# Optimization experiments

Measured on AMD Instinct MI355X. Metric: run time of the kernel, lower is better.

## Reference

```python
import jax, jax.numpy as jnp
import numpy as np

PATCH = (9, 7, 5, 3)
DIM = 64
HEAD_DIM = 64
HEADS = 8
HIDDEN = 8
DEPTH = 4
SCALE = (HEAD_DIM / HEADS) ** (-0.5)  # per-head dim = 8
EPS = 1e-5


def setup_inputs() -> dict:
    key = jax.random.key(0)
    ks = jax.random.split(key, 8)
    B = 4096
    x = jax.random.normal(ks[0], (B, PATCH[0] * PATCH[0], DIM), dtype=jnp.float32)
    w_qkv = jax.random.normal(ks[1], (DEPTH, DIM, 3 * HEAD_DIM), dtype=jnp.float32) * 0.05
    b_qkv = jnp.zeros((DEPTH, 3 * HEAD_DIM), dtype=jnp.float32)
    w_o = jax.random.normal(ks[2], (DEPTH, HEAD_DIM, DIM), dtype=jnp.float32) * 0.05
    b_o = jnp.zeros((DEPTH, DIM), dtype=jnp.float32)
    ln1_g = jnp.ones((DEPTH, DIM), dtype=jnp.float32)
    ln1_b = jnp.zeros((DEPTH, DIM), dtype=jnp.float32)
    ln2_g = jnp.ones((DEPTH, DIM), dtype=jnp.float32)
    ln2_b = jnp.zeros((DEPTH, DIM), dtype=jnp.float32)
    w1 = jax.random.normal(ks[3], (DEPTH, DIM, HIDDEN), dtype=jnp.float32) * 0.05
    b1 = jnp.zeros((DEPTH, HIDDEN), dtype=jnp.float32)
    w2 = jax.random.normal(ks[4], (DEPTH, HIDDEN, DIM), dtype=jnp.float32) * 0.05
    b2 = jnp.zeros((DEPTH, DIM), dtype=jnp.float32)
    return {"x": x, "w_qkv": w_qkv, "b_qkv": b_qkv, "w_o": w_o, "b_o": b_o,
            "ln1_g": ln1_g, "ln1_b": ln1_b, "ln2_g": ln2_g, "ln2_b": ln2_b,
            "w1": w1, "b1": b1, "w2": w2, "b2": b2}


def _layernorm(x, g, b):
    m = jnp.mean(x, axis=-1, keepdims=True)
    v = jnp.mean(jnp.square(x - m), axis=-1, keepdims=True)
    return (x - m) * jax.lax.rsqrt(v + EPS) * g + b


def reference(x, w_qkv, b_qkv, w_o, b_o, ln1_g, ln1_b, ln2_g, ln2_b, w1, b1, w2, b2):
    B = x.shape[0]
    for i in range(DEPTH):
        n = x.shape[1]
        # --- attention block (Residual(Layernorm(Encoder))) ---
        y = _layernorm(x, ln1_g[i], ln1_b[i])
        qkv = y @ w_qkv[i] + b_qkv[i]                       # [B, n, 3*HEAD_DIM]
        q, k, v = jnp.split(qkv, 3, axis=-1)
        dh = HEAD_DIM // HEADS                              # 8
        q = q.reshape(B, n, HEADS, dh)
        k = k.reshape(B, n, HEADS, dh)
        v = v.reshape(B, n, HEADS, dh)
        dots = jnp.einsum('bihd,bjhd->bhij', q, k) * SCALE  # [B, H, n, n]
        attn = jax.nn.softmax(dots, axis=-1)
        out = jnp.einsum('bhij,bjhd->bihd', attn, v).reshape(B, n, HEAD_DIM)
        out = out @ w_o[i] + b_o[i]
        x = x + out                                         # dropout = identity (eval)
        # --- feedforward block ---
        y = _layernorm(x, ln2_g[i], ln2_b[i])
        h = jax.nn.gelu(y @ w1[i] + b1[i], approximate=False)
        x = x + h @ w2[i] + b2[i]
        # --- spatial pooling / rearrange ---
        p = PATCH[i]
        xg = x.reshape(B, p, p, DIM)                        # 'b (h w) d -> b h w d'
        if i != DEPTH - 1:
            xg = xg[:, 1:-1, 1:-1, :]                       # crop pool_size=1
            x = xg.reshape(B, (p - 2) * (p - 2), DIM)
        else:
            x = jnp.transpose(xg, (0, 3, 1, 2))             # 'b h w d -> b d h w'
    return x  # [B, 64, 3, 3]
```

## Files before the change

### kernel.cpp

```cpp
#include <hip/hip_runtime.h>
#include <hip/hip_bf16.h>
#include <math.h>

#define NT 512

typedef __attribute__((ext_vector_type(8))) short short8v;
typedef __attribute__((ext_vector_type(4))) short short4v;
typedef __attribute__((ext_vector_type(4))) float f32x4;
typedef __attribute__((ext_vector_type(2))) unsigned uint2v;
typedef __attribute__((ext_vector_type(4))) unsigned uint4v;

__device__ __forceinline__ unsigned short f2bf(float x) {
    unsigned u = __float_as_uint(x);
    unsigned r = ((u >> 16) & 1u) + 0x7FFFu;
    return (unsigned short)((u + r) >> 16);
}
__device__ __forceinline__ unsigned pk2(float a, float b) {
    __hip_bfloat162 h = __float22bfloat162_rn(make_float2(a, b));
    unsigned r;
    __builtin_memcpy(&r, &h, sizeof(r));
    return r;
}
__device__ __forceinline__ short bf1(float a) {
    __hip_bfloat16 h = __float2bfloat16(a);
    short r;
    __builtin_memcpy(&r, &h, sizeof(r));
    return r;
}
__device__ __forceinline__ float exp2fast(float x) {
#if __has_builtin(__builtin_amdgcn_exp2f)
    return __builtin_amdgcn_exp2f(x);
#else
    return exp2f(x);
#endif
}
__device__ __forceinline__ float gelu_f(float x) {
    float x3 = x * x * x;
    float e = exp2fast(-2.3022079f * x - 0.1029432f * x3);
    return x / (1.0f + e);
}
__device__ __forceinline__ f32x4 mfma32(short8v a, short8v b, f32x4 c) {
    return __builtin_amdgcn_mfma_f32_16x16x32_bf16(a, b, c, 0, 0, 0);
}

#define WS_WO 49152
#define WS_W1 65536
#define WS_W2 69632
#define WS_TOT 71680

__global__ __launch_bounds__(256) void prep_kernel(
    const float* __restrict__ w_qkv, const float* __restrict__ w_o,
    const float* __restrict__ w1, const float* __restrict__ w2,
    short* __restrict__ ws)
{
    int idx = blockIdx.x * 256 + threadIdx.x;
    if (idx < WS_WO) {
        int l = idx / 12288, r = idx % 12288, c = r >> 6, d = r & 63;
        ws[idx] = (short)f2bf(w_qkv[l * 12288 + d * 192 + c]);
    } else if (idx < WS_W1) {
        int k = idx - WS_WO; int l = k / 4096, r = k % 4096, c = r >> 6, d = r & 63;
        ws[idx] = (short)f2bf(w_o[l * 4096 + d * 64 + c]);
    } else if (idx < WS_W2) {
        int k = idx - WS_W1; int l = k / 1024, r = k % 1024, j = r >> 6, d = r & 63;
        ws[idx] = (j < 8) ? (short)f2bf(w1[l * 512 + d * 8 + j]) : (short)0;
    } else if (idx < WS_TOT) {
        int k = idx - WS_W2; int l = k / 512, r = k % 512, c = r >> 3, j = r & 7;
        ws[idx] = (short)f2bf(w2[l * 512 + j * 64 + c]);
    }
}

template<int N, int P, int L, bool LAST>
__device__ __forceinline__ void layer_fn(
    float* __restrict__ xs, short* __restrict__ ybf, short* __restrict__ qbf,
    short* __restrict__ kbf, short* __restrict__ vT,
    const short* __restrict__ ws,
    const float* __restrict__ b_qkv, const float* __restrict__ b_o,
    const float* __restrict__ ln1_g, const float* __restrict__ ln1_b,
    const float* __restrict__ ln2_g, const float* __restrict__ ln2_b,
    const float* __restrict__ b1,    const float* __restrict__ b2,
    float* __restrict__ out, int b, int t)
{
    constexpr int Mt = (N + 15) / 16;
    constexpr float SCL2E = 0.51010905835f;
    const int wv = t >> 6, l = t & 63, lr = l & 15, lq = l >> 4;
    short8v zero8 = {};
    f32x4 zero4 = {0.f, 0.f, 0.f, 0.f};

    if (t < 64 * Mt) {
        const int token = t >> 2, part = t & 3, d0 = part * 16;
        short* yrow = ybf + token * 72 + d0;
        if (token < N) {
            const int row = (token / P + L) * 9 + token % P + L;
            const float* xr = xs + row * 68 + d0;
            f32x4 v[4];
            #pragma unroll
            for (int k = 0; k < 4; ++k) v[k] = *(const f32x4*)(xr + 4 * k);
            float s1 = 0.f, s2 = 0.f;
            #pragma unroll
            for (int k = 0; k < 4; ++k)
                #pragma unroll
                for (int e = 0; e < 4; ++e) { s1 += v[k][e]; s2 += v[k][e] * v[k][e]; }
            s1 += __shfl_xor(s1, 1); s2 += __shfl_xor(s2, 1);
            s1 += __shfl_xor(s1, 2); s2 += __shfl_xor(s2, 2);
            const float m = s1 * 0.015625f;
            const float r = rsqrtf(s2 * 0.015625f - m * m + 1e-5f);
            uint4v w0, w1v;
            #pragma unroll
            for (int k = 0; k < 4; ++k) {
                f32x4 g  = *(const f32x4*)&ln1_g[L * 64 + d0 + 4 * k];
                f32x4 bb = *(const f32x4*)&ln1_b[L * 64 + d0 + 4 * k];
                unsigned p0 = pk2((v[k][0]-m)*r*g[0]+bb[0], (v[k][1]-m)*r*g[1]+bb[1]);
                unsigned p1 = pk2((v[k][2]-m)*r*g[2]+bb[2], (v[k][3]-m)*r*g[3]+bb[3]);
                if (k == 0) { w0.x = p0; w0.y = p1; }
                else if (k == 1) { w0.z = p0; w0.w = p1; }
                else if (k == 2) { w1v.x = p0; w1v.y = p1; }
                else { w1v.z = p0; w1v.w = p1; }
            }
            *(uint4v*)yrow = w0;
            *(uint4v*)(yrow + 8) = w1v;
        } else {
            uint4v z = {};
            *(uint4v*)yrow = z;
            *(uint4v*)(yrow + 8) = z;
        }
    }
    __syncthreads();

    {
        const short* wqL = ws + L * 12288;
        for (int u = wv; u < Mt * 12; u += 8) {
            const int mt = u / 12, ct = u - mt * 12;
            const short* yr = &ybf[(16 * mt + lr) * 72 + lq * 8];
            short8v y0 = *(const short8v*)yr, y1 = *(const short8v*)(yr + 32);
            const short* wr = &wqL[(16 * ct + lr) * 64 + lq * 8];
            short8v w0 = *(const short8v*)wr, w1 = *(const short8v*)(wr + 32);
            if (ct < 8) {
                f32x4 acc = mfma32(w0, y0, zero4);
                acc = mfma32(w1, y1, acc);
                f32x4 bq = *(const f32x4*)&b_qkv[L * 192 + 16 * ct + lq * 4];
                const int i = 16 * mt + lr;
                if (ct < 4) {
                    unsigned p0 = pk2((acc[0]+bq[0])*SCL2E, (acc[1]+bq[1])*SCL2E);
                    unsigned p1 = pk2((acc[2]+bq[2])*SCL2E, (acc[3]+bq[3])*SCL2E);
                    unsigned* dst = (unsigned*)&qbf[i * 72 + 16 * ct + lq * 4];
                    dst[0] = p0; dst[1] = p1;
                } else {
                    unsigned p0 = pk2(acc[0]+bq[0], acc[1]+bq[1]);
                    unsigned p1 = pk2(acc[2]+bq[2], acc[3]+bq[3]);
                    unsigned* dst = (unsigned*)&kbf[i * 72 + 16 * (ct - 4) + lq * 4];
                    dst[0] = p0; dst[1] = p1;
                }
            } else {
                f32x4 acc = mfma32(y0, w0, zero4);
                acc = mfma32(y1, w1, acc);
                const int cv = 16 * (ct - 8) + lr;
                const float bias = b_qkv[L * 192 + 128 + cv];
                unsigned p0 = pk2(acc[0]+bias, acc[1]+bias);
                unsigned p1 = pk2(acc[2]+bias, acc[3]+bias);
                unsigned* dst = (unsigned*)&vT[cv * 104 + 16 * mt + lq * 4];
                dst[0] = p0; dst[1] = p1;
            }
        }
    }
    __syncthreads();

    {
        const int h = wv, hh = wv >> 1;
        short8v kf[Mt];
        #pragma unroll
        for (int jt = 0; jt < Mt; ++jt)
            kf[jt] = (l < 16) ? *(const short8v*)&kbf[(16 * jt + lr) * 72 + h * 8] : zero8;
#if __has_builtin(__builtin_amdgcn_mfma_f32_16x16x16bf16_1k)
        short4v vf[Mt];
        #pragma unroll
        for (int jt = 0; jt < Mt; ++jt)
            vf[jt] = *(const short4v*)&vT[(16 * hh + lr) * 104 + 16 * jt + lq * 4];
#else
        constexpr int KS2 = (Mt + 1) / 2;
        short8v vf8[KS2];
        #pragma unroll
        for (int ks = 0; ks < KS2; ++ks)
            vf8[ks] = *(const short8v*)&vT[(16 * hh + lr) * 104 + 32 * ks + lq * 8];
#endif
        for (int mt = 0; mt < Mt; ++mt) {
            short8v bq = (l < 16) ? *(const short8v*)&qbf[(16 * mt + lr) * 72 + h * 8] : zero8;
            f32x4 acc[Mt];
            #pragma unroll
            for (int jt = 0; jt < Mt; ++jt) acc[jt] = mfma32(kf[jt], bq, zero4);
            float psum = 0.f;
            #pragma unroll
            for (int jt = 0; jt < Mt; ++jt) {
                #pragma unroll
                for (int rg = 0; rg < 4; ++rg) {
                    const int j = 16 * jt + lq * 4 + rg;
                    float e = exp2fast(acc[jt][rg]);
                    e = (j < N) ? e : 0.f;
                    acc[jt][rg] = e;
                    psum += e;
                }
            }
            float den = psum + __shfl_xor(psum, 16);
            den += __shfl_xor(den, 32);
            const float dinv = 1.0f / den;
            unsigned pkk[Mt][2];
            #pragma unroll
            for (int jt = 0; jt < Mt; ++jt) {
                pkk[jt][0] = pk2(acc[jt][0] * dinv, acc[jt][1] * dinv);
                pkk[jt][1] = pk2(acc[jt][2] * dinv, acc[jt][3] * dinv);
            }
            f32x4 po = zero4;
#if __has_builtin(__builtin_amdgcn_mfma_f32_16x16x16bf16_1k)
            #pragma unroll
            for (int jt = 0; jt < Mt; ++jt) {
                uint2v pw; pw.x = pkk[jt][0]; pw.y = pkk[jt][1];
                short4v bv = __builtin_bit_cast(short4v, pw);
                po = __builtin_amdgcn_mfma_f32_16x16x16bf16_1k(vf[jt], bv, po, 0, 0, 0);
            }
#else
            #pragma unroll
            for (int ks = 0; ks < KS2; ++ks) {
                const int t1ok = (2 * ks + 1) < Mt;
                unsigned pA0 = pkk[2 * ks][0], pA1 = pkk[2 * ks][1];
                unsigned pB0 = t1ok ? pkk[2 * ks + 1][0] : 0u;
                unsigned pB1 = t1ok ? pkk[2 * ks + 1][1] : 0u;
                int i01 = ((((lq & 1) * 2) * 16) + lr) * 4;
                int i23 = ((((lq & 1) * 2 + 1) * 16) + lr) * 4;
                unsigned w0a = (unsigned)__builtin_amdgcn_ds_bpermute(i01, (int)pA0);
                unsigned w0b = (unsigned)__builtin_amdgcn_ds_bpermute(i01, (int)pB0);
                unsigned w1a = (unsigned)__builtin_amdgcn_ds_bpermute(i01, (int)pA1);
                unsigned w1b = (unsigned)__builtin_amdgcn_ds_bpermute(i01, (int)pB1);
                unsigned w2a = (unsigned)__builtin_amdgcn_ds_bpermute(i23, (int)pA0);
                unsigned w2b = (unsigned)__builtin_amdgcn_ds_bpermute(i23, (int)pB0);
                unsigned w3a = (unsigned)__builtin_amdgcn_ds_bpermute(i23, (int)pA1);
                unsigned w3b = (unsigned)__builtin_amdgcn_ds_bpermute(i23, (int)pB1);
                uint4v wv4;
                wv4.x = (lq >> 1) ? w0b : w0a;
                wv4.y = (lq >> 1) ? w1b : w1a;
                wv4.z = (lq >> 1) ? w2b : w2a;
                wv4.w = (lq >> 1) ? w3b : w3a;
                short8v bv = __builtin_bit_cast(short8v, wv4);
                po = mfma32(vf8[ks], bv, po);
            }
#endif
            if ((lq >> 1) == (h & 1)) {
                const int i = 16 * mt + lr;
                if (i < N) {
                    unsigned q0 = pk2(po[0], po[1]);
                    unsigned q1 = pk2(po[2], po[3]);
                    unsigned* dst = (unsigned*)&ybf[i * 72 + h * 8 + (lq & 1) * 4];
                    dst[0] = q0; dst[1] = q1;
                }
            }
        }
    }
    __syncthreads();

    {
        short* hb = qbf;
        if (wv < Mt) {
            const int mt = wv;
            const int i = 16 * mt + lr;
            const bool iok = (i < N);
            const int xrow = iok ? (i / P + L) * 9 + (i % P) + L : 0;
            float* xp = xs + xrow * 68;
            const short* yr = &ybf[i * 72 + lq * 8];
            short8v y0 = *(const short8v*)yr;
            short8v y1 = *(const short8v*)(yr + 32);
            const short* woL = ws + WS_WO + L * 4096;
            f32x4 xv[4];
            float s1 = 0.f, s2 = 0.f;
            #pragma unroll
            for (int ct = 0; ct < 4; ++ct) {
                const short* wr = &woL[(16 * ct + lr) * 64 + lq * 8];
                short8v w0 = *(const short8v*)wr, w1 = *(const short8v*)(wr + 32);
                f32x4 acc = mfma32(w0, y0, zero4);
                acc = mfma32(w1, y1, acc);
                f32x4 bo = *(const f32x4*)&b_o[L * 64 + 16 * ct + 4 * lq];
                f32x4 xc = zero4;
                if (iok) xc = *(const f32x4*)(xp + 16 * ct + 4 * lq);
                #pragma unroll
                for (int rg = 0; rg < 4; ++rg) {
                    xc[rg] += acc[rg] + bo[rg];
                    s1 += xc[rg]; s2 += xc[rg] * xc[rg];
                }
                if (iok) *(f32x4*)(xp + 16 * ct + 4 * lq) = xc;
                xv[ct] = xc;
            }
            s1 += __shfl_xor(s1, 16); s2 += __shfl_xor(s2, 16);
            s1 += __shfl_xor(s1, 32); s2 += __shfl_xor(s2, 32);
            const float m = s1 * 0.015625f;
            const float r = rsqrtf(s2 * 0.015625f - m * m + 1e-5f);
            unsigned* ybw = (unsigned*)&ybf[i * 72];
            #pragma unroll
            for (int ct = 0; ct < 4; ++ct) {
                f32x4 g  = *(const f32x4*)&ln2_g[L * 64 + 16 * ct + 4 * lq];
                f32x4 bb = *(const f32x4*)&ln2_b[L * 64 + 16 * ct + 4 * lq];
                ybw[8 * ct + 2 * lq]     = pk2((xv[ct][0]-m)*r*g[0]+bb[0],
                                               (xv[ct][1]-m)*r*g[1]+bb[1]);
                ybw[8 * ct + 2 * lq + 1] = pk2((xv[ct][2]-m)*r*g[2]+bb[2],
                                               (xv[ct][3]-m)*r*g[3]+bb[3]);
            }
            uint4v ua0 = *(const uint4v*)(ybw + 4 * lq);
            uint4v ua1 = *(const uint4v*)(ybw + 16 + 4 * lq);
            const short* w1L = ws + WS_W1 + L * 1024;
            short8v a10 = __builtin_bit_cast(short8v, ua0);
            short8v a11 = __builtin_bit_cast(short8v, ua1);
            short8v b10 = *(const short8v*)&w1L[lr * 64 + lq * 8];
            short8v b11 = *(const short8v*)&w1L[lr * 64 + lq * 8 + 32];
            f32x4 hA = mfma32(a10, b10, zero4);
            hA = mfma32(a11, b11, hA);
            const float bg = (lr < 8) ? b1[L * 8 + lr] : 0.f;
            if (lr < 8) {
                #pragma unroll
                for (int rg = 0; rg < 4; ++rg)
                    hb[(16 * mt + 4 * lq + rg) * 8 + lr] = bf1(gelu_f(hA[rg] + bg));
            }
            short8v ah = (lq == 0) ? *(const short8v*)&hb[(16 * mt + lr) * 8] : zero8;
            int row2[4]; bool ok2[4];
            #pragma unroll
            for (int rg = 0; rg < 4; ++rg) {
                const int i2 = 16 * mt + 4 * lq + rg;
                ok2[rg] = (i2 < N);
                row2[rg] = ok2[rg] ? (i2 / P + L) * 9 + (i2 % P) + L : 0;
            }
            const short* w2L = ws + WS_W2 + L * 512;
            #pragma unroll
            for (int ct = 0; ct < 4; ++ct) {
                short8v bw2 = (lq == 0) ? *(const short8v*)&w2L[(16 * ct + lr) * 8] : zero8;
                f32x4 dacc = mfma32(ah, bw2, zero4);
                const int c2 = 16 * ct + lr;
                const float b2v = b2[L * 64 + c2];
                #pragma unroll
                for (int rg = 0; rg < 4; ++rg)
                    if (ok2[rg]) xs[row2[rg] * 68 + c2] += dacc[rg] + b2v;
            }
        }
    }
    __syncthreads();

    if (LAST) {
        for (int idx = t; idx < 576; idx += NT) {
            const int d = idx / 9, rc = idx % 9;
            const int row = (rc / 3 + 3) * 9 + rc % 3 + 3;
            out[(size_t)b * 576 + idx] = xs[row * 68 + d];
        }
    }
}

__global__ __launch_bounds__(NT, 4) void vit_kernel(
    const float* __restrict__ x_in, const short* __restrict__ ws,
    const float* __restrict__ b_qkv, const float* __restrict__ b_o,
    const float* __restrict__ ln1_g, const float* __restrict__ ln1_b,
    const float* __restrict__ ln2_g, const float* __restrict__ ln2_b,
    const float* __restrict__ b1,    const float* __restrict__ b2,
    float* __restrict__ out)
{
    __shared__ __align__(16) float xs[81 * 68];
    __shared__ __align__(16) short ybf[96 * 72];
    __shared__ __align__(16) short qbf[96 * 72];
    __shared__ __align__(16) short kbf[96 * 72];
    __shared__ __align__(16) short vT[64 * 104];

    const int b = blockIdx.x;
    const int t = threadIdx.x;

    for (int idx = t; idx < 64 * 104; idx += NT) vT[idx] = 0;

    const float* xin = x_in + (size_t)b * 5184;
    for (int q4 = t; q4 < 1296; q4 += NT) {
        const int i = q4 >> 4, dq = q4 & 15;
        *(f32x4*)&xs[i * 68 + dq * 4] = *(const f32x4*)&xin[i * 64 + dq * 4];
    }
    __syncthreads();

    layer_fn<81, 9, 0, false>(xs, ybf, qbf, kbf, vT, ws, b_qkv, b_o,
                              ln1_g, ln1_b, ln2_g, ln2_b, b1, b2, out, b, t);
    layer_fn<49, 7, 1, false>(xs, ybf, qbf, kbf, vT, ws, b_qkv, b_o,
                              ln1_g, ln1_b, ln2_g, ln2_b, b1, b2, out, b, t);
    layer_fn<25, 5, 2, false>(xs, ybf, qbf, kbf, vT, ws, b_qkv, b_o,
                              ln1_g, ln1_b, ln2_g, ln2_b, b1, b2, out, b, t);
    layer_fn<9, 3, 3, true>(xs, ybf, qbf, kbf, vT, ws, b_qkv, b_o,
                            ln1_g, ln1_b, ln2_g, ln2_b, b1, b2, out, b, t);
}

extern "C" void kernel_launch(void* const* d_in, const int* in_sizes, int n_in,
                              void* d_out, int out_size, void* d_ws, size_t ws_size,
                              hipStream_t stream) {
    (void)n_in; (void)out_size; (void)ws_size;
    const float* x     = (const float*)d_in[0];
    const float* w_qkv = (const float*)d_in[1];
    const float* b_qkv = (const float*)d_in[2];
    const float* w_o   = (const float*)d_in[3];
    const float* b_o   = (const float*)d_in[4];
    const float* ln1_g = (const float*)d_in[5];
    const float* ln1_b = (const float*)d_in[6];
    const float* ln2_g = (const float*)d_in[7];
    const float* ln2_b = (const float*)d_in[8];
    const float* w1    = (const float*)d_in[9];
    const float* b1    = (const float*)d_in[10];
    const float* w2    = (const float*)d_in[11];
    const float* b2    = (const float*)d_in[12];
    short* ws = (short*)d_ws;

    prep_kernel<<<dim3((WS_TOT + 255) / 256), dim3(256), 0, stream>>>(w_qkv, w_o, w1, w2, ws);

    int B = in_sizes[0] / (81 * 64);
    vit_kernel<<<dim3(B), dim3(NT), 0, stream>>>(
        x, ws, b_qkv, b_o, ln1_g, ln1_b, ln2_g, ln2_b, b1, b2, (float*)d_out);
}
```

Baseline: 400.2 us.

## Fuse next-layer LN1 into FFN epilogue and ping-pong y/V buffers

Keeps the FFN output in registers and computes the next layer's LayerNorm1 directly in the FFN epilogue. It writes that result into an alternating buffer that doubles as the V-transpose storage, so the separate LN1 pass and one barrier per layer are dropped. The softmax normalisation is deferred to after the PV MFMA, using two accumulators to split the dependency chain, and the reductions use tree sums. The main risk is that the ping-pong aliasing of vbuf/ybf with different strides (72 vs 104) and the padding zeroing must stay correct across layers.

```diff
diff --git a/kernel.cpp b/kernel.cpp
--- a/kernel.cpp
+++ b/kernel.cpp
@@ -41,6 +41,35 @@
 }
 __device__ __forceinline__ f32x4 mfma32(short8v a, short8v b, f32x4 c) {
     return __builtin_amdgcn_mfma_f32_16x16x32_bf16(a, b, c, 0, 0, 0);
+}
+
+template<int M>
+__device__ __forceinline__ float sum_tree(const f32x4* a) {
+    float p[M];
+    #pragma unroll
+    for (int i = 0; i < M; ++i)
+        p[i] = (a[i][0] + a[i][1]) + (a[i][2] + a[i][3]);
+    #pragma unroll
+    for (int s = 1; s < M; s *= 2)
+        #pragma unroll
+        for (int i = 0; i + s < M; i += 2 * s) p[i] += p[i + s];
+    return p[0];
+}
+template<int M>
+__device__ __forceinline__ void stats_tree(const f32x4* v, float& s1o, float& s2o) {
+    float a[M], b[M];
+    #pragma unroll
+    for (int i = 0; i < M; ++i) {
+        a[i] = (v[i][0] + v[i][1]) + (v[i][2] + v[i][3]);
+        float q0 = v[i][0] * v[i][0], q1 = v[i][1] * v[i][1];
+        float q2 = v[i][2] * v[i][2], q3 = v[i][3] * v[i][3];
+        b[i] = (q0 + q1) + (q2 + q3);
+    }
+    #pragma unroll
+    for (int s = 1; s < M; s *= 2)
+        #pragma unroll
+        for (int i = 0; i + s < M; i += 2 * s) { a[i] += a[i + s]; b[i] += b[i + s]; }
+    s1o = a[0]; s2o = b[0];
 }
 
 #define WS_WO 49152
@@ -69,10 +98,10 @@
     }
 }
 
-template<int N, int P, int L, bool LAST>
+template<int N, int P, int L, bool FIRST, bool LAST>
 __device__ __forceinline__ void layer_fn(
-    float* __restrict__ xs, short* __restrict__ ybf, short* __restrict__ qbf,
-    short* __restrict__ kbf, short* __restrict__ vT,
+    float* __restrict__ xs, short* __restrict__ y, short* __restrict__ vb,
+    short* __restrict__ qbf, short* __restrict__ kbf,
     const short* __restrict__ ws,
     const float* __restrict__ b_qkv, const float* __restrict__ b_o,
     const float* __restrict__ ln1_g, const float* __restrict__ ln1_b,
@@ -86,51 +115,50 @@
     short8v zero8 = {};
     f32x4 zero4 = {0.f, 0.f, 0.f, 0.f};
 
-    if (t < 64 * Mt) {
-        const int token = t >> 2, part = t & 3, d0 = part * 16;
-        short* yrow = ybf + token * 72 + d0;
-        if (token < N) {
-            const int row = (token / P + L) * 9 + token % P + L;
-            const float* xr = xs + row * 68 + d0;
-            f32x4 v[4];
-            #pragma unroll
-            for (int k = 0; k < 4; ++k) v[k] = *(const f32x4*)(xr + 4 * k);
-            float s1 = 0.f, s2 = 0.f;
-            #pragma unroll
-            for (int k = 0; k < 4; ++k)
-                #pragma unroll
-                for (int e = 0; e < 4; ++e) { s1 += v[k][e]; s2 += v[k][e] * v[k][e]; }
-            s1 += __shfl_xor(s1, 1); s2 += __shfl_xor(s2, 1);
-            s1 += __shfl_xor(s1, 2); s2 += __shfl_xor(s2, 2);
-            const float m = s1 * 0.015625f;
-            const float r = rsqrtf(s2 * 0.015625f - m * m + 1e-5f);
-            uint4v w0, w1v;
-            #pragma unroll
-            for (int k = 0; k < 4; ++k) {
-                f32x4 g  = *(const f32x4*)&ln1_g[L * 64 + d0 + 4 * k];
-                f32x4 bb = *(const f32x4*)&ln1_b[L * 64 + d0 + 4 * k];
-                unsigned p0 = pk2((v[k][0]-m)*r*g[0]+bb[0], (v[k][1]-m)*r*g[1]+bb[1]);
-                unsigned p1 = pk2((v[k][2]-m)*r*g[2]+bb[2], (v[k][3]-m)*r*g[3]+bb[3]);
-                if (k == 0) { w0.x = p0; w0.y = p1; }
-                else if (k == 1) { w0.z = p0; w0.w = p1; }
-                else if (k == 2) { w1v.x = p0; w1v.y = p1; }
-                else { w1v.z = p0; w1v.w = p1; }
-            }
-            *(uint4v*)yrow = w0;
-            *(uint4v*)(yrow + 8) = w1v;
-        } else {
-            uint4v z = {};
-            *(uint4v*)yrow = z;
-            *(uint4v*)(yrow + 8) = z;
+    if (FIRST) {
+        if (t < 64 * Mt) {
+            const int token = t >> 2, part = t & 3, d0 = part * 16;
+            short* yrow = y + token * 72 + d0;
+            if (token < N) {
+                const int row = (token / P + L) * 9 + token % P + L;
+                const float* xr = xs + row * 68 + d0;
+                f32x4 v[4];
+                #pragma unroll
+                for (int k = 0; k < 4; ++k) v[k] = *(const f32x4*)(xr + 4 * k);
+                float s1, s2;
+                stats_tree<4>(v, s1, s2);
+                s1 += __shfl_xor(s1, 1); s2 += __shfl_xor(s2, 1);
+                s1 += __shfl_xor(s1, 2); s2 += __shfl_xor(s2, 2);
+                const float m = s1 * 0.015625f;
+                const float r = rsqrtf(s2 * 0.015625f - m * m + 1e-5f);
+                uint4v w0, w1v;
+                #pragma unroll
+                for (int k = 0; k < 4; ++k) {
+                    f32x4 g  = *(const f32x4*)&ln1_g[L * 64 + d0 + 4 * k];
+                    f32x4 bb = *(const f32x4*)&ln1_b[L * 64 + d0 + 4 * k];
+                    unsigned p0 = pk2((v[k][0]-m)*r*g[0]+bb[0], (v[k][1]-m)*r*g[1]+bb[1]);
+                    unsigned p1 = pk2((v[k][2]-m)*r*g[2]+bb[2], (v[k][3]-m)*r*g[3]+bb[3]);
+                    if (k == 0) { w0.x = p0; w0.y = p1; }
+                    else if (k == 1) { w0.z = p0; w0.w = p1; }
+                    else if (k == 2) { w1v.x = p0; w1v.y = p1; }
+                    else { w1v.z = p0; w1v.w = p1; }
+                }
+                *(uint4v*)yrow = w0;
+                *(uint4v*)(yrow + 8) = w1v;
+            } else {
+                uint4v z = {};
+                *(uint4v*)yrow = z;
+                *(uint4v*)(yrow + 8) = z;
+            }
         }
-    }
-    __syncthreads();
+        __syncthreads();
+    }
 
     {
         const short* wqL = ws + L * 12288;
         for (int u = wv; u < Mt * 12; u += 8) {
             const int mt = u / 12, ct = u - mt * 12;
-            const short* yr = &ybf[(16 * mt + lr) * 72 + lq * 8];
+            const short* yr = &y[(16 * mt + lr) * 72 + lq * 8];
             short8v y0 = *(const short8v*)yr, y1 = *(const short8v*)(yr + 32);
             const short* wr = &wqL[(16 * ct + lr) * 64 + lq * 8];
             short8v w0 = *(const short8v*)wr, w1 = *(const short8v*)(wr + 32);
@@ -157,7 +185,7 @@
                 const float bias = b_qkv[L * 192 + 128 + cv];
                 unsigned p0 = pk2(acc[0]+bias, acc[1]+bias);
                 unsigned p1 = pk2(acc[2]+bias, acc[3]+bias);
-                unsigned* dst = (unsigned*)&vT[cv * 104 + 16 * mt + lq * 4];
+                unsigned* dst = (unsigned*)&vb[cv * 104 + 16 * mt + lq * 4];
                 dst[0] = p0; dst[1] = p1;
             }
         }
@@ -174,47 +202,49 @@
         short4v vf[Mt];
         #pragma unroll
         for (int jt = 0; jt < Mt; ++jt)
-            vf[jt] = *(const short4v*)&vT[(16 * hh + lr) * 104 + 16 * jt + lq * 4];
+            vf[jt] = *(const short4v*)&vb[(16 * hh + lr) * 104 + 16 * jt + lq * 4];
 #else
         constexpr int KS2 = (Mt + 1) / 2;
         short8v vf8[KS2];
         #pragma unroll
         for (int ks = 0; ks < KS2; ++ks)
-            vf8[ks] = *(const short8v*)&vT[(16 * hh + lr) * 104 + 32 * ks + lq * 8];
+            vf8[ks] = *(const short8v*)&vb[(16 * hh + lr) * 104 + 32 * ks + lq * 8];
 #endif
         for (int mt = 0; mt < Mt; ++mt) {
             short8v bq = (l < 16) ? *(const short8v*)&qbf[(16 * mt + lr) * 72 + h * 8] : zero8;
             f32x4 acc[Mt];
             #pragma unroll
             for (int jt = 0; jt < Mt; ++jt) acc[jt] = mfma32(kf[jt], bq, zero4);
-            float psum = 0.f;
             #pragma unroll
             for (int jt = 0; jt < Mt; ++jt) {
                 #pragma unroll
                 for (int rg = 0; rg < 4; ++rg) {
-                    const int j = 16 * jt + lq * 4 + rg;
                     float e = exp2fast(acc[jt][rg]);
-                    e = (j < N) ? e : 0.f;
+                    if (jt == Mt - 1) {
+                        const int j = 16 * jt + lq * 4 + rg;
+                        e = (j < N) ? e : 0.f;
+                    }
                     acc[jt][rg] = e;
-                    psum += e;
                 }
             }
+            float psum = sum_tree<Mt>(acc);
             float den = psum + __shfl_xor(psum, 16);
             den += __shfl_xor(den, 32);
             const float dinv = 1.0f / den;
             unsigned pkk[Mt][2];
             #pragma unroll
             for (int jt = 0; jt < Mt; ++jt) {
-                pkk[jt][0] = pk2(acc[jt][0] * dinv, acc[jt][1] * dinv);
-                pkk[jt][1] = pk2(acc[jt][2] * dinv, acc[jt][3] * dinv);
-            }
-            f32x4 po = zero4;
+                pkk[jt][0] = pk2(acc[jt][0], acc[jt][1]);
+                pkk[jt][1] = pk2(acc[jt][2], acc[jt][3]);
+            }
+            f32x4 po0 = zero4, po1 = zero4;
 #if __has_builtin(__builtin_amdgcn_mfma_f32_16x16x16bf16_1k)
             #pragma unroll
             for (int jt = 0; jt < Mt; ++jt) {
                 uint2v pw; pw.x = pkk[jt][0]; pw.y = pkk[jt][1];
                 short4v bv = __builtin_bit_cast(short4v, pw);
-                po = __builtin_amdgcn_mfma_f32_16x16x16bf16_1k(vf[jt], bv, po, 0, 0, 0);
+                if (jt & 1) po1 = __builtin_amdgcn_mfma_f32_16x16x16bf16_1k(vf[jt], bv, po1, 0, 0, 0);
+                else        po0 = __builtin_amdgcn_mfma_f32_16x16x16bf16_1k(vf[jt], bv, po0, 0, 0, 0);
             }
 #else
             #pragma unroll
@@ -239,15 +269,15 @@
                 wv4.z = (lq >> 1) ? w2b : w2a;
                 wv4.w = (lq >> 1) ? w3b : w3a;
                 short8v bv = __builtin_bit_cast(short8v, wv4);
-                po = mfma32(vf8[ks], bv, po);
+                po0 = mfma32(vf8[ks], bv, po0);
             }
 #endif
             if ((lq >> 1) == (h & 1)) {
                 const int i = 16 * mt + lr;
                 if (i < N) {
-                    unsigned q0 = pk2(po[0], po[1]);
-                    unsigned q1 = pk2(po[2], po[3]);
-                    unsigned* dst = (unsigned*)&ybf[i * 72 + h * 8 + (lq & 1) * 4];
+                    unsigned q0 = pk2((po0[0]+po1[0])*dinv, (po0[1]+po1[1])*dinv);
+                    unsigned q1 = pk2((po0[2]+po1[2])*dinv, (po0[3]+po1[3])*dinv);
+                    unsigned* dst = (unsigned*)&y[i * 72 + h * 8 + (lq & 1) * 4];
                     dst[0] = q0; dst[1] = q1;
                 }
             }
@@ -263,34 +293,30 @@
             const bool iok = (i < N);
             const int xrow = iok ? (i / P + L) * 9 + (i % P) + L : 0;
             float* xp = xs + xrow * 68;
-            const short* yr = &ybf[i * 72 + lq * 8];
+            const short* yr = &y[i * 72 + lq * 8];
             short8v y0 = *(const short8v*)yr;
             short8v y1 = *(const short8v*)(yr + 32);
             const short* woL = ws + WS_WO + L * 4096;
             f32x4 xv[4];
-            float s1 = 0.f, s2 = 0.f;
             #pragma unroll
             for (int ct = 0; ct < 4; ++ct) {
                 const short* wr = &woL[(16 * ct + lr) * 64 + lq * 8];
-                short8v w0 = *(const short8v*)wr, w1 = *(const short8v*)(wr + 32);
-                f32x4 acc = mfma32(w0, y0, zero4);
-                acc = mfma32(w1, y1, acc);
+                f32x4 acc = mfma32(*(const short8v*)wr, y0, zero4);
+                acc = mfma32(*(const short8v*)(wr + 32), y1, acc);
                 f32x4 bo = *(const f32x4*)&b_o[L * 64 + 16 * ct + 4 * lq];
                 f32x4 xc = zero4;
                 if (iok) xc = *(const f32x4*)(xp + 16 * ct + 4 * lq);
                 #pragma unroll
-                for (int rg = 0; rg < 4; ++rg) {
-                    xc[rg] += acc[rg] + bo[rg];
-                    s1 += xc[rg]; s2 += xc[rg] * xc[rg];
-                }
-                if (iok) *(f32x4*)(xp + 16 * ct + 4 * lq) = xc;
+                for (int rg = 0; rg < 4; ++rg) xc[rg] += acc[rg] + bo[rg];
                 xv[ct] = xc;
             }
+            float s1, s2;
+            stats_tree<4>(xv, s1, s2);
             s1 += __shfl_xor(s1, 16); s2 += __shfl_xor(s2, 16);
             s1 += __shfl_xor(s1, 32); s2 += __shfl_xor(s2, 32);
             const float m = s1 * 0.015625f;
             const float r = rsqrtf(s2 * 0.015625f - m * m + 1e-5f);
-            unsigned* ybw = (unsigned*)&ybf[i * 72];
+            unsigned* ybw = (unsigned*)&y[i * 72];
             #pragma unroll
             for (int ct = 0; ct < 4; ++ct) {
                 f32x4 g  = *(const f32x4*)&ln2_g[L * 64 + 16 * ct + 4 * lq];
@@ -309,31 +335,52 @@
             short8v b11 = *(const short8v*)&w1L[lr * 64 + lq * 8 + 32];
             f32x4 hA = mfma32(a10, b10, zero4);
             hA = mfma32(a11, b11, hA);
-            const float bg = (lr < 8) ? b1[L * 8 + lr] : 0.f;
             if (lr < 8) {
+                const float bg = b1[L * 8 + lr];
                 #pragma unroll
                 for (int rg = 0; rg < 4; ++rg)
                     hb[(16 * mt + 4 * lq + rg) * 8 + lr] = bf1(gelu_f(hA[rg] + bg));
             }
-            short8v ah = (lq == 0) ? *(const short8v*)&hb[(16 * mt + lr) * 8] : zero8;
-            int row2[4]; bool ok2[4];
-            #pragma unroll
-            for (int rg = 0; rg < 4; ++rg) {
-                const int i2 = 16 * mt + 4 * lq + rg;
-                ok2[rg] = (i2 < N);
-                row2[rg] = ok2[rg] ? (i2 / P + L) * 9 + (i2 % P) + L : 0;
-            }
+            short8v hbf = (lq == 0) ? *(const short8v*)&hb[(16 * mt + lr) * 8] : zero8;
             const short* w2L = ws + WS_W2 + L * 512;
+            f32x4 xf[4];
             #pragma unroll
             for (int ct = 0; ct < 4; ++ct) {
-                short8v bw2 = (lq == 0) ? *(const short8v*)&w2L[(16 * ct + lr) * 8] : zero8;
-                f32x4 dacc = mfma32(ah, bw2, zero4);
-                const int c2 = 16 * ct + lr;
-                const float b2v = b2[L * 64 + c2];
-                #pragma unroll
-                for (int rg = 0; rg < 4; ++rg)
-                    if (ok2[rg]) xs[row2[rg] * 68 + c2] += dacc[rg] + b2v;
-            }
+                short8v a2 = (lq == 0) ? *(const short8v*)&w2L[(16 * ct + lr) * 8] : zero8;
+                f32x4 dacc = mfma32(a2, hbf, zero4);
+                f32x4 b2v = *(const f32x4*)&b2[L * 64 + 16 * ct + 4 * lq];
+                #pragma unroll
+                for (int rg = 0; rg < 4; ++rg) xf[ct][rg] = xv[ct][rg] + dacc[rg] + b2v[rg];
+                if (iok) *(f32x4*)(xp + 16 * ct + 4 * lq) = xf[ct];
+            }
+            if (!LAST) {
+                float t1, t2;
+                stats_tree<4>(xf, t1, t2);
+                t1 += __shfl_xor(t1, 16); t2 += __shfl_xor(t2, 16);
+                t1 += __shfl_xor(t1, 32); t2 += __shfl_xor(t2, 32);
+                const float mn = t1 * 0.015625f;
+                const float rn = rsqrtf(t2 * 0.015625f - mn * mn + 1e-5f);
+                const int r_ = i / P, c_ = i % P;
+                const bool vok = iok && r_ >= 1 && r_ <= P - 2 && c_ >= 1 && c_ <= P - 2;
+                if (vok) {
+                    const int j = (r_ - 1) * (P - 2) + (c_ - 1);
+                    unsigned* yw = (unsigned*)&vb[j * 72];
+                    #pragma unroll
+                    for (int ct = 0; ct < 4; ++ct) {
+                        f32x4 g  = *(const f32x4*)&ln1_g[(L + 1) * 64 + 16 * ct + 4 * lq];
+                        f32x4 bb = *(const f32x4*)&ln1_b[(L + 1) * 64 + 16 * ct + 4 * lq];
+                        yw[8 * ct + 2 * lq]     = pk2((xf[ct][0]-mn)*rn*g[0]+bb[0],
+                                                      (xf[ct][1]-mn)*rn*g[1]+bb[1]);
+                        yw[8 * ct + 2 * lq + 1] = pk2((xf[ct][2]-mn)*rn*g[2]+bb[2],
+                                                      (xf[ct][3]-mn)*rn*g[3]+bb[3]);
+                    }
+                }
+            }
+        } else if (!LAST && wv == Mt) {
+            constexpr int Pn = P - 2, Nn = Pn * Pn, Mtn = (Nn + 15) / 16;
+            constexpr int PadU = (16 * Mtn - Nn) * 36;
+            unsigned* zb = (unsigned*)(vb + Nn * 72);
+            for (int z = l; z < PadU; z += 64) zb[z] = 0;
         }
     }
     __syncthreads();
@@ -357,14 +404,14 @@
 {
     __shared__ __align__(16) float xs[81 * 68];
     __shared__ __align__(16) short ybf[96 * 72];
+    __shared__ __align__(16) short vbuf[64 * 104];
     __shared__ __align__(16) short qbf[96 * 72];
     __shared__ __align__(16) short kbf[96 * 72];
-    __shared__ __align__(16) short vT[64 * 104];
 
     const int b = blockIdx.x;
     const int t = threadIdx.x;
 
-    for (int idx = t; idx < 64 * 104; idx += NT) vT[idx] = 0;
+    for (int idx = t; idx < 64 * 104; idx += NT) vbuf[idx] = 0;
 
     const float* xin = x_in + (size_t)b * 5184;
     for (int q4 = t; q4 < 1296; q4 += NT) {
@@ -373,14 +420,14 @@
     }
     __syncthreads();
 
-    layer_fn<81, 9, 0, false>(xs, ybf, qbf, kbf, vT, ws, b_qkv, b_o,
-                              ln1_g, ln1_b, ln2_g, ln2_b, b1, b2, out, b, t);
-    layer_fn<49, 7, 1, false>(xs, ybf, qbf, kbf, vT, ws, b_qkv, b_o,
-                              ln1_g, ln1_b, ln2_g, ln2_b, b1, b2, out, b, t);
-    layer_fn<25, 5, 2, false>(xs, ybf, qbf, kbf, vT, ws, b_qkv, b_o,
-                              ln1_g, ln1_b, ln2_g, ln2_b, b1, b2, out, b, t);
-    layer_fn<9, 3, 3, true>(xs, ybf, qbf, kbf, vT, ws, b_qkv, b_o,
-                            ln1_g, ln1_b, ln2_g, ln2_b, b1, b2, out, b, t);
+    layer_fn<81, 9, 0, true,  false>(xs, ybf,  vbuf, qbf, kbf, ws, b_qkv, b_o,
+                                     ln1_g, ln1_b, ln2_g, ln2_b, b1, b2, out, b, t);
+    layer_fn<49, 7, 1, false, false>(xs, vbuf, ybf,  qbf, kbf, ws, b_qkv, b_o,
+                                     ln1_g, ln1_b, ln2_g, ln2_b, b1, b2, out, b, t);
+    layer_fn<25, 5, 2, false, false>(xs, ybf,  vbuf, qbf, kbf, ws, b_qkv, b_o,
+                                     ln1_g, ln1_b, ln2_g, ln2_b, b1, b2, out, b, t);
+    layer_fn<9,  3, 3, false, true >(xs, vbuf, ybf,  qbf, kbf, ws, b_qkv, b_o,
+                                     ln1_g, ln1_b, ln2_g, ln2_b, b1, b2, out, b, t);
 }
 
 extern "C" void kernel_launch(void* const* d_in, const int* in_sizes, int n_in,
```

New measurement: 377.2 us. -5.8%, faster.
